# Kernel optimization log

Measured on AMD Instinct MI355X. Metric: run time of the kernel, lower is better.

## Reference

```python
import jax, jax.numpy as jnp
import numpy as np

B, S = 4, 2048
D_MODEL, N_HEADS, D_KV = 1024, 16, 64
NUM_BUCKETS, MAX_DIST = 32, 128


def _relative_position_bucket(relative_position, num_buckets=NUM_BUCKETS, max_distance=MAX_DIST):
    # bidirectional (encoder) variant, faithful to FlaxT5Attention._relative_position_bucket
    num_buckets = num_buckets // 2
    relative_buckets = (relative_position > 0).astype(jnp.int32) * num_buckets
    rp = jnp.abs(relative_position)
    max_exact = num_buckets // 2
    is_small = rp < max_exact
    rp_large = max_exact + (
        jnp.log(rp.astype(jnp.float32) / max_exact)
        / np.log(max_distance / max_exact)
        * (num_buckets - max_exact)
    )
    rp_large = jnp.minimum(rp_large, num_buckets - 1)
    return relative_buckets + jnp.where(is_small, rp, rp_large.astype(jnp.int32))


def setup_inputs() -> dict:
    key = jax.random.key(0)
    ks = jax.random.split(key, 6)
    return {
        "hidden_states": jax.random.normal(ks[0], (B, S, D_MODEL), jnp.float32),
        "mask": jnp.zeros((B, S), jnp.float32),  # additive mask, 0 = attend
        "wq": jax.random.normal(ks[1], (D_MODEL, N_HEADS * D_KV), jnp.float32) * 0.02,
        "wk": jax.random.normal(ks[2], (D_MODEL, N_HEADS * D_KV), jnp.float32) * 0.02,
        "wv": jax.random.normal(ks[3], (D_MODEL, N_HEADS * D_KV), jnp.float32) * 0.02,
        "wo": jax.random.normal(ks[4], (N_HEADS * D_KV, D_MODEL), jnp.float32) * 0.02,
        "rel_bias": jax.random.normal(ks[5], (NUM_BUCKETS, N_HEADS), jnp.float32) * 0.02,
    }


def reference(hidden_states, mask, wq, wk, wv, wo, rel_bias):
    b, s, _ = hidden_states.shape
    # QKV projections, split heads -> [B, S, H, D]
    q = (hidden_states @ wq).reshape(b, s, N_HEADS, D_KV)
    k = (hidden_states @ wk).reshape(b, s, N_HEADS, D_KV)
    v = (hidden_states @ wv).reshape(b, s, N_HEADS, D_KV)

    # relative position bias -> [1, H, S, S]
    pos = jnp.arange(s, dtype=jnp.int32)
    relative_position = pos[None, :] - pos[:, None]  # memory - query
    buckets = _relative_position_bucket(relative_position)
    position_bias = rel_bias[buckets].transpose(2, 0, 1)[None]  # [1,H,S,S]
    # encoder path: additive mask expanded to [B,1,1,K]
    position_bias = position_bias + mask[:, None, None, :]

    # flax dot_product_attention_weights scales q by 1/sqrt(depth)
    scores = jnp.einsum("bqhd,bkhd->bhqk", q / jnp.sqrt(jnp.float32(D_KV)), k)
    attn_weights = jax.nn.softmax(scores + position_bias, axis=-1)

    attn_output = jnp.einsum("bhqk,bkhd->bqhd", attn_weights, v)
    attn_output = attn_output.reshape(b, s, N_HEADS * D_KV) @ wo
    return attn_output, position_bias
```

## Files before the change

kernel.cpp:

```cpp
#include <hip/hip_runtime.h>
#include <hip/hip_bf16.h>

typedef __attribute__((ext_vector_type(8))) short bf16x8;
typedef __attribute__((ext_vector_type(8))) unsigned short u16x8;
typedef __attribute__((ext_vector_type(4))) float f32x4;

#define B_   4
#define S_   2048
#define H_   16
#define DKV  64
#define DM   1024

static __device__ __forceinline__ f32x4 mfma16(bf16x8 a, bf16x8 b, f32x4 c){
  return __builtin_amdgcn_mfma_f32_16x16x32_bf16(a, b, c, 0, 0, 0);
}
static __device__ __forceinline__ void gload_lds16(const void* g, void* l){
  __builtin_amdgcn_global_load_lds((const __attribute__((address_space(1))) void*)g,
                                   (__attribute__((address_space(3))) void*)l, 16, 0, 0);
}
static __device__ __forceinline__ unsigned short f2b(float f){
  union { __hip_bfloat16 b; unsigned short u; } x;
  x.b = __float2bfloat16(f);
  return x.u;
}

__global__ void cast_h_kernel(const float* __restrict__ in, unsigned short* __restrict__ out, int n4){
  int i = blockIdx.x * 256 + threadIdx.x;
  if (i >= n4) return;
  float4 v = reinterpret_cast<const float4*>(in)[i];
  ushort4 r;
  r.x = f2b(v.x); r.y = f2b(v.y); r.z = f2b(v.z); r.w = f2b(v.w);
  reinterpret_cast<ushort4*>(out)[i] = r;
}

__global__ void transpose_w_kernel(const float* __restrict__ w0, const float* __restrict__ w1,
                                   const float* __restrict__ w2, const float* __restrict__ w3,
                                   unsigned short* o0, unsigned short* o1,
                                   unsigned short* o2, unsigned short* o3){
  int z = blockIdx.z;
  const float* src = (z==0) ? w0 : (z==1) ? w1 : (z==2) ? w2 : w3;
  unsigned short* dst = (z==0) ? o0 : (z==1) ? o1 : (z==2) ? o2 : o3;
  __shared__ float tile[32][33];
  int bx = blockIdx.x * 32, by = blockIdx.y * 32;
  int tx = threadIdx.x, ty = threadIdx.y;
  #pragma unroll
  for (int i = 0; i < 32; i += 8)
    tile[ty + i][tx] = src[(size_t)(by + ty + i) * DM + bx + tx];
  __syncthreads();
  #pragma unroll
  for (int i = 0; i < 32; i += 8)
    dst[(size_t)(bx + ty + i) * DM + by + tx] = f2b(tile[tx][ty + i]);
}

__global__ void build_table_kernel(const float* __restrict__ rel_bias, float* __restrict__ table_t){
  int i = blockIdx.x * 256 + threadIdx.x;
  if (i >= 16 * 4095) return;
  int h = i / 4095;
  int idx = i - h * 4095;
  int rel = idx - 2047;
  int bucket = (rel > 0) ? 16 : 0;
  int rp = (rel < 0) ? -rel : rel;
  int off;
  if (rp < 8) off = rp;
  else off = 8 + (rp>=12) + (rp>=16) + (rp>=23) + (rp>=32) + (rp>=46) + (rp>=64) + (rp>=91);
  table_t[i] = rel_bias[(bucket + off) * 16 + h];
}

__global__ void posbias_kernel(const float* __restrict__ relb, const float* __restrict__ mask,
                               float* __restrict__ out){
  __shared__ float rbh[32];
  int row = blockIdx.x;
  int q = row & (S_ - 1);
  int h = (row >> 11) & (H_ - 1);
  int b = row >> 15;
  int tid = threadIdx.x;
  if (tid < 32) rbh[tid] = relb[tid * 16 + h];
  __syncthreads();
  const float* mrow = mask + b * S_;
  float* orow = out + (size_t)row * S_;
  int k0 = tid * 8;
  #pragma unroll
  for (int c = 0; c < 2; ++c){
    float4 mv = *(const float4*)(mrow + k0 + c * 4);
    float4 v;
    #pragma unroll
    for (int j = 0; j < 4; ++j){
      int k = k0 + c * 4 + j;
      int rel = k - q;
      int bucket = (rel > 0) ? 16 : 0;
      int rp = (rel < 0) ? -rel : rel;
      int off = (rp < 8) ? rp
              : 8 + (rp>=12) + (rp>=16) + (rp>=23) + (rp>=32) + (rp>=46) + (rp>=64) + (rp>=91);
      (&v.x)[j] = rbh[bucket + off] + (&mv.x)[j];
    }
    *(float4*)(orow + k0 + c*4) = v;
  }
}

template<int MODE>
__global__ __launch_bounds__(256, 2) void gemm_bt_kernel(
    const unsigned short* __restrict__ A, const unsigned short* __restrict__ Bt,
    void* __restrict__ outp, int M, int N, int K, float scale)
{
  __shared__ __align__(16) unsigned short As[2][128 * 32];
  __shared__ __align__(16) unsigned short Bs[2][128 * 32];
  int tid = threadIdx.x; int lane = tid & 63; int w = tid >> 6;
  int wr = w >> 1, wc = w & 1;
  int n0 = blockIdx.x * 128, m0 = blockIdx.y * 128;
  const char* Ab = (const char*)A;
  const char* Bb = (const char*)Bt;
  size_t Kb = (size_t)K * 2;

  f32x4 acc[4][4];
  #pragma unroll
  for (int i = 0; i < 4; ++i)
    #pragma unroll
    for (int j = 0; j < 4; ++j) acc[i][j] = (f32x4){0.f, 0.f, 0.f, 0.f};

  auto stage = [&](int kt, int bsel){
    size_t k0b = (size_t)kt * 64;
    #pragma unroll
    for (int c = 0; c < 2; ++c){
      int o = c * 4096 + w * 1024 + lane * 16;
      int row = o >> 6;
      int wbl = (o & 63) ^ (((row >> 1) & 3) << 4);
      gload_lds16(Ab + (size_t)(m0 + row) * Kb + k0b + wbl, (char*)As[bsel] + c * 4096 + w * 1024);
      gload_lds16(Bb + (size_t)(n0 + row) * Kb + k0b + wbl, (char*)Bs[bsel] + c * 4096 + w * 1024);
    }
  };

  int nk = K >> 5;
  int buf = 0;
  stage(0, 0);
  for (int kt = 0; kt < nk; ++kt){
    __syncthreads();
    if (kt + 1 < nk) stage(kt + 1, buf ^ 1);
    bf16x8 af[4], bfr[4];
    #pragma unroll
    for (int f = 0; f < 4; ++f){
      int row = wr * 64 + f * 16 + (lane & 15);
      int byt = (row * 64 + ((lane >> 4) * 16)) ^ (((row >> 1) & 3) << 4);
      af[f] = *(const bf16x8*)((const char*)As[buf] + byt);
    }
    #pragma unroll
    for (int f = 0; f < 4; ++f){
      int row = wc * 64 + f * 16 + (lane & 15);
      int byt = (row * 64 + ((lane >> 4) * 16)) ^ (((row >> 1) & 3) << 4);
      bfr[f] = *(const bf16x8*)((const char*)Bs[buf] + byt);
    }
    #pragma unroll
    for (int i = 0; i < 4; ++i)
      #pragma unroll
      for (int j = 0; j < 4; ++j)
        acc[i][j] = mfma16(af[i], bfr[j], acc[i][j]);
    buf ^= 1;
  }

  #pragma unroll
  for (int i = 0; i < 4; ++i){
    #pragma unroll
    for (int j = 0; j < 4; ++j){
      #pragma unroll
      for (int r = 0; r < 4; ++r){
        int m = m0 + wr * 64 + i * 16 + ((lane >> 4) * 4) + r;
        int n = n0 + wc * 64 + j * 16 + (lane & 15);
        if (MODE == 0){
          ((float*)outp)[(size_t)m * N + n] = acc[i][j][r] * scale;
        } else {
          int sel = n >> 10, nn = n & 1023;
          float v = acc[i][j][r] * (sel == 0 ? 0.125f : 1.0f);
          int b = m >> 11, s = m & 2047, hh = nn >> 6, d = nn & 63;
          ((unsigned short*)outp)[(size_t)sel * 8388608 +
              (((size_t)(b * H_ + hh) * S_) + s) * DKV + d] = f2b(v);
        }
      }
    }
  }
}

__global__ __launch_bounds__(256, 2) void attn_mfma_kernel(
    const unsigned short* __restrict__ Qp, const unsigned short* __restrict__ Kp,
    const unsigned short* __restrict__ Vp, const float* __restrict__ table_t,
    const float* __restrict__ mask, unsigned short* __restrict__ outp)
{
  __shared__ __align__(16) unsigned short Ks[64][72];
  __shared__ __align__(16) unsigned short Vs[64][72];
  __shared__ __align__(16) unsigned short Ps[4][16][72];
  __shared__ float bias_s[127];
  __shared__ float mask_s[64];

  int bid = blockIdx.x;
  int qt = bid & 31; int h = (bid >> 5) & 15; int b = bid >> 9;
  int qb = qt * 64;
  const unsigned short* qptr = Qp + ((size_t)(b * H_ + h) * S_ + qb) * DKV;
  const unsigned short* kptr = Kp + (size_t)(b * H_ + h) * S_ * DKV;
  const unsigned short* vptr = Vp + (size_t)(b * H_ + h) * S_ * DKV;
  int tid = threadIdx.x; int lane = tid & 63; int w = tid >> 6;

  bf16x8 qf[2];
  {
    const unsigned short* qrow = qptr + (size_t)(w * 16 + (lane & 15)) * DKV + 8 * (lane >> 4);
    qf[0] = *(const bf16x8*)qrow;
    qf[1] = *(const bf16x8*)(qrow + 32);
  }
  float l_r[4] = {0.f, 0.f, 0.f, 0.f};
  f32x4 o_acc[4];
  #pragma unroll
  for (int d = 0; d < 4; ++d) o_acc[d] = (f32x4){0.f, 0.f, 0.f, 0.f};

  int bias_base = h * 4095 + (2047 - qb - 63);

  int skey = tid & 63;
  int sd0  = (tid >> 6) * 16;

  u16x8 ka, kb2, va, vb2;
  float biasr = 0.f, maskr = 0.f;
  auto gload = [&](int k0){
    const unsigned short* krow = kptr + (size_t)(k0 + skey) * DKV + sd0;
    const unsigned short* vrow = vptr + (size_t)(k0 + skey) * DKV + sd0;
    ka  = *(const u16x8*)krow;
    kb2 = *(const u16x8*)(krow + 8);
    va  = *(const u16x8*)vrow;
    vb2 = *(const u16x8*)(vrow + 8);
    if (tid < 127) biasr = table_t[bias_base + k0 + tid];
    else if (tid >= 128 && tid < 192) maskr = mask[b * S_ + k0 + (tid - 128)];
  };
  auto lwrite = [&](){
    *(u16x8*)&Ks[skey][sd0]     = ka;
    *(u16x8*)&Ks[skey][sd0 + 8] = kb2;
    #pragma unroll
    for (int j = 0; j < 8; ++j){
      Vs[sd0 + j][skey]     = va[j];
      Vs[sd0 + 8 + j][skey] = vb2[j];
    }
    if (tid < 127) bias_s[tid] = biasr;
    else if (tid < 192) mask_s[tid - 128] = maskr;
  };

  gload(0);
  lwrite();
  for (int k0 = 0; k0 < S_; k0 += 64){
    __syncthreads();
    if (k0 + 64 < S_) gload(k0 + 64);

    f32x4 sc[4];
    #pragma unroll
    for (int kb = 0; kb < 4; ++kb){
      sc[kb] = (f32x4){0.f, 0.f, 0.f, 0.f};
      #pragma unroll
      for (int ks = 0; ks < 2; ++ks){
        int row = kb * 16 + (lane & 15);
        bf16x8 kf = *(const bf16x8*)&Ks[row][ks * 32 + (lane >> 4) * 8];
        sc[kb] = mfma16(qf[ks], kf, sc[kb]);
      }
    }
    float t[4][4];
    float rs[4] = {0.f, 0.f, 0.f, 0.f};
    #pragma unroll
    for (int kb = 0; kb < 4; ++kb){
      int k_l = kb * 16 + (lane & 15);
      float mk = mask_s[k_l];
      #pragma unroll
      for (int r = 0; r < 4; ++r){
        int q_l = w * 16 + (lane >> 4) * 4 + r;
        float p = __expf(sc[kb][r] + bias_s[k_l - q_l + 63] + mk);
        t[kb][r] = p;
        rs[r] += p;
      }
    }
    #pragma unroll
    for (int r = 0; r < 4; ++r){
      #pragma unroll
      for (int off = 1; off < 16; off <<= 1)
        rs[r] += __shfl_xor(rs[r], off, 64);
      l_r[r] += rs[r];
    }
    #pragma unroll
    for (int kb = 0; kb < 4; ++kb)
      #pragma unroll
      for (int r = 0; r < 4; ++r){
        int prow = (lane >> 4) * 4 + r;
        int pcol = kb * 16 + (lane & 15);
        Ps[w][prow][pcol] = f2b(t[kb][r]);
      }
    bf16x8 pa[2];
    #pragma unroll
    for (int ks = 0; ks < 2; ++ks)
      pa[ks] = *(const bf16x8*)&Ps[w][lane & 15][ks * 32 + (lane >> 4) * 8];
    #pragma unroll
    for (int db = 0; db < 4; ++db)
      #pragma unroll
      for (int ks = 0; ks < 2; ++ks){
        bf16x8 vf = *(const bf16x8*)&Vs[db * 16 + (lane & 15)][ks * 32 + (lane >> 4) * 8];
        o_acc[db] = mfma16(pa[ks], vf, o_acc[db]);
      }

    __syncthreads();
    if (k0 + 64 < S_) lwrite();
  }

  #pragma unroll
  for (int r = 0; r < 4; ++r){
    float inv = 1.0f / l_r[r];
    int qg = qb + w * 16 + (lane >> 4) * 4 + r;
    size_t rowoff = ((size_t)b * S_ + qg) * DM + h * DKV;
    #pragma unroll
    for (int db = 0; db < 4; ++db)
      outp[rowoff + db * 16 + (lane & 15)] = f2b(o_acc[db][r] * inv);
  }
}

extern "C" void kernel_launch(void* const* d_in, const int* in_sizes, int n_in,
                              void* d_out, int out_size, void* d_ws, size_t ws_size,
                              hipStream_t stream) {
  const float* hs   = (const float*)d_in[0];
  const float* msk  = (const float*)d_in[1];
  const float* wq   = (const float*)d_in[2];
  const float* wk   = (const float*)d_in[3];
  const float* wv   = (const float*)d_in[4];
  const float* wo   = (const float*)d_in[5];
  const float* relb = (const float*)d_in[6];

  float* out_attn = (float*)d_out;
  float* out_pb   = (float*)d_out + (size_t)B_ * S_ * DM;

  const size_t SCRATCH_NEED = 76021760;
  char* ws = (ws_size >= SCRATCH_NEED && d_ws) ? (char*)d_ws : (char*)out_pb;

  unsigned short* h_bf  = (unsigned short*)(ws + 0);
  unsigned short* wqkv_t= (unsigned short*)(ws + 16777216);
  unsigned short* wk_t  = (unsigned short*)(ws + 18874368);
  unsigned short* wv_t  = (unsigned short*)(ws + 20971520);
  unsigned short* wo_t  = (unsigned short*)(ws + 23068672);
  unsigned short* qkv_b = (unsigned short*)(ws + 25165824);
  unsigned short* k_b   = (unsigned short*)(ws + 41943040);
  unsigned short* v_b   = (unsigned short*)(ws + 58720256);
  float*          tabl  = (float*)(ws + 75497472);

  cast_h_kernel<<<8192, 256, 0, stream>>>(hs, h_bf, (B_ * S_ * DM) / 4);
  transpose_w_kernel<<<dim3(32, 32, 4), dim3(32, 8), 0, stream>>>(wq, wk, wv, wo,
                                                                  wqkv_t, wk_t, wv_t, wo_t);
  build_table_kernel<<<256, 256, 0, stream>>>(relb, tabl);

  gemm_bt_kernel<1><<<dim3(24, 64), 256, 0, stream>>>(h_bf, wqkv_t, qkv_b, 8192, 3072, 1024, 1.0f);

  attn_mfma_kernel<<<B_ * H_ * 32, 256, 0, stream>>>(qkv_b, k_b, v_b, tabl, msk, h_bf);

  gemm_bt_kernel<0><<<dim3(8, 64), 256, 0, stream>>>(h_bf, wo_t, out_attn, 8192, 1024, 1024, 1.0f);

  posbias_kernel<<<B_ * H_ * S_, 256, 0, stream>>>(relb, msk, out_pb);
}
```

Baseline: 502.2 us.

## Process 32 query rows per wave in attention to reuse K/V tiles

The attention kernel now covers 128 queries per block instead of 64, so each wave handles two 16-row query sub-tiles. K and V fragments are loaded from LDS into registers once and reused for both sub-tiles, which halves LDS and global K/V traffic per query. The bias window grows to 191 entries to match. In exchange the grid shrinks to 1024 blocks and register pressure rises, which may lower occupancy under launch_bounds(256,2).

```diff
diff --git a/kernel.cpp b/kernel.cpp
--- a/kernel.cpp
+++ b/kernel.cpp
@@ -185,30 +185,33 @@
 {
   __shared__ __align__(16) unsigned short Ks[64][72];
   __shared__ __align__(16) unsigned short Vs[64][72];
-  __shared__ __align__(16) unsigned short Ps[4][16][72];
-  __shared__ float bias_s[127];
+  __shared__ __align__(16) unsigned short Ps[4][32][72];
+  __shared__ float bias_s[191];
   __shared__ float mask_s[64];
 
   int bid = blockIdx.x;
-  int qt = bid & 31; int h = (bid >> 5) & 15; int b = bid >> 9;
-  int qb = qt * 64;
+  int qt = bid & 15; int h = (bid >> 4) & 15; int b = bid >> 8;
+  int qb = qt * 128;
   const unsigned short* qptr = Qp + ((size_t)(b * H_ + h) * S_ + qb) * DKV;
   const unsigned short* kptr = Kp + (size_t)(b * H_ + h) * S_ * DKV;
   const unsigned short* vptr = Vp + (size_t)(b * H_ + h) * S_ * DKV;
   int tid = threadIdx.x; int lane = tid & 63; int w = tid >> 6;
 
-  bf16x8 qf[2];
-  {
-    const unsigned short* qrow = qptr + (size_t)(w * 16 + (lane & 15)) * DKV + 8 * (lane >> 4);
-    qf[0] = *(const bf16x8*)qrow;
-    qf[1] = *(const bf16x8*)(qrow + 32);
-  }
-  float l_r[4] = {0.f, 0.f, 0.f, 0.f};
-  f32x4 o_acc[4];
-  #pragma unroll
-  for (int d = 0; d < 4; ++d) o_acc[d] = (f32x4){0.f, 0.f, 0.f, 0.f};
-
-  int bias_base = h * 4095 + (2047 - qb - 63);
+  bf16x8 qf[2][2];
+  #pragma unroll
+  for (int qs = 0; qs < 2; ++qs){
+    const unsigned short* qrow = qptr + (size_t)(w * 32 + qs * 16 + (lane & 15)) * DKV + 8 * (lane >> 4);
+    qf[qs][0] = *(const bf16x8*)qrow;
+    qf[qs][1] = *(const bf16x8*)(qrow + 32);
+  }
+  float l_r[2][4] = {{0.f,0.f,0.f,0.f},{0.f,0.f,0.f,0.f}};
+  f32x4 o_acc[2][4];
+  #pragma unroll
+  for (int qs = 0; qs < 2; ++qs)
+    #pragma unroll
+    for (int d = 0; d < 4; ++d) o_acc[qs][d] = (f32x4){0.f, 0.f, 0.f, 0.f};
+
+  int bias_base = h * 4095 + (2047 - qb - 127);
 
   int skey = tid & 63;
   int sd0  = (tid >> 6) * 16;
@@ -222,8 +225,8 @@
     kb2 = *(const u16x8*)(krow + 8);
     va  = *(const u16x8*)vrow;
     vb2 = *(const u16x8*)(vrow + 8);
-    if (tid < 127) biasr = table_t[bias_base + k0 + tid];
-    else if (tid >= 128 && tid < 192) maskr = mask[b * S_ + k0 + (tid - 128)];
+    if (tid < 191) biasr = table_t[bias_base + k0 + tid];
+    else if (tid >= 192) maskr = mask[b * S_ + k0 + (tid - 192)];
   };
   auto lwrite = [&](){
     *(u16x8*)&Ks[skey][sd0]     = ka;
@@ -233,8 +236,8 @@
       Vs[sd0 + j][skey]     = va[j];
       Vs[sd0 + 8 + j][skey] = vb2[j];
     }
-    if (tid < 127) bias_s[tid] = biasr;
-    else if (tid < 192) mask_s[tid - 128] = maskr;
+    if (tid < 191) bias_s[tid] = biasr;
+    else if (tid >= 192) mask_s[tid - 192] = maskr;
   };
 
   gload(0);
@@ -243,71 +246,89 @@
     __syncthreads();
     if (k0 + 64 < S_) gload(k0 + 64);
 
-    f32x4 sc[4];
-    #pragma unroll
-    for (int kb = 0; kb < 4; ++kb){
-      sc[kb] = (f32x4){0.f, 0.f, 0.f, 0.f};
-      #pragma unroll
-      for (int ks = 0; ks < 2; ++ks){
-        int row = kb * 16 + (lane & 15);
-        bf16x8 kf = *(const bf16x8*)&Ks[row][ks * 32 + (lane >> 4) * 8];
-        sc[kb] = mfma16(qf[ks], kf, sc[kb]);
+    bf16x8 kf[4][2];
+    #pragma unroll
+    for (int kb = 0; kb < 4; ++kb)
+      #pragma unroll
+      for (int ks = 0; ks < 2; ++ks)
+        kf[kb][ks] = *(const bf16x8*)&Ks[kb * 16 + (lane & 15)][ks * 32 + (lane >> 4) * 8];
+
+    float t[2][4][4];
+    float rs[2][4] = {{0.f,0.f,0.f,0.f},{0.f,0.f,0.f,0.f}};
+    #pragma unroll
+    for (int qs = 0; qs < 2; ++qs){
+      f32x4 sc[4];
+      #pragma unroll
+      for (int kb = 0; kb < 4; ++kb){
+        sc[kb] = (f32x4){0.f, 0.f, 0.f, 0.f};
+        #pragma unroll
+        for (int ks = 0; ks < 2; ++ks)
+          sc[kb] = mfma16(qf[qs][ks], kf[kb][ks], sc[kb]);
       }
-    }
-    float t[4][4];
-    float rs[4] = {0.f, 0.f, 0.f, 0.f};
-    #pragma unroll
-    for (int kb = 0; kb < 4; ++kb){
-      int k_l = kb * 16 + (lane & 15);
-      float mk = mask_s[k_l];
+      #pragma unroll
+      for (int kb = 0; kb < 4; ++kb){
+        int k_l = kb * 16 + (lane & 15);
+        float mk = mask_s[k_l];
+        #pragma unroll
+        for (int r = 0; r < 4; ++r){
+          int q_l = w * 32 + qs * 16 + (lane >> 4) * 4 + r;
+          float p = __expf(sc[kb][r] + bias_s[k_l - q_l + 127] + mk);
+          t[qs][kb][r] = p;
+          rs[qs][r] += p;
+        }
+      }
+    }
+    #pragma unroll
+    for (int qs = 0; qs < 2; ++qs)
       #pragma unroll
       for (int r = 0; r < 4; ++r){
-        int q_l = w * 16 + (lane >> 4) * 4 + r;
-        float p = __expf(sc[kb][r] + bias_s[k_l - q_l + 63] + mk);
-        t[kb][r] = p;
-        rs[r] += p;
+        #pragma unroll
+        for (int off = 1; off < 16; off <<= 1)
+          rs[qs][r] += __shfl_xor(rs[qs][r], off, 64);
+        l_r[qs][r] += rs[qs][r];
       }
-    }
-    #pragma unroll
-    for (int r = 0; r < 4; ++r){
-      #pragma unroll
-      for (int off = 1; off < 16; off <<= 1)
-        rs[r] += __shfl_xor(rs[r], off, 64);
-      l_r[r] += rs[r];
-    }
-    #pragma unroll
-    for (int kb = 0; kb < 4; ++kb)
-      #pragma unroll
-      for (int r = 0; r < 4; ++r){
-        int prow = (lane >> 4) * 4 + r;
-        int pcol = kb * 16 + (lane & 15);
-        Ps[w][prow][pcol] = f2b(t[kb][r]);
-      }
-    bf16x8 pa[2];
-    #pragma unroll
-    for (int ks = 0; ks < 2; ++ks)
-      pa[ks] = *(const bf16x8*)&Ps[w][lane & 15][ks * 32 + (lane >> 4) * 8];
+    #pragma unroll
+    for (int qs = 0; qs < 2; ++qs)
+      #pragma unroll
+      for (int kb = 0; kb < 4; ++kb)
+        #pragma unroll
+        for (int r = 0; r < 4; ++r)
+          Ps[w][qs * 16 + (lane >> 4) * 4 + r][kb * 16 + (lane & 15)] = f2b(t[qs][kb][r]);
+
+    bf16x8 vf[4][2];
     #pragma unroll
     for (int db = 0; db < 4; ++db)
       #pragma unroll
-      for (int ks = 0; ks < 2; ++ks){
-        bf16x8 vf = *(const bf16x8*)&Vs[db * 16 + (lane & 15)][ks * 32 + (lane >> 4) * 8];
-        o_acc[db] = mfma16(pa[ks], vf, o_acc[db]);
-      }
+      for (int ks = 0; ks < 2; ++ks)
+        vf[db][ks] = *(const bf16x8*)&Vs[db * 16 + (lane & 15)][ks * 32 + (lane >> 4) * 8];
+    #pragma unroll
+    for (int qs = 0; qs < 2; ++qs){
+      bf16x8 pa[2];
+      #pragma unroll
+      for (int ks = 0; ks < 2; ++ks)
+        pa[ks] = *(const bf16x8*)&Ps[w][qs * 16 + (lane & 15)][ks * 32 + (lane >> 4) * 8];
+      #pragma unroll
+      for (int db = 0; db < 4; ++db)
+        #pragma unroll
+        for (int ks = 0; ks < 2; ++ks)
+          o_acc[qs][db] = mfma16(pa[ks], vf[db][ks], o_acc[qs][db]);
+    }
 
     __syncthreads();
     if (k0 + 64 < S_) lwrite();
   }
 
   #pragma unroll
-  for (int r = 0; r < 4; ++r){
-    float inv = 1.0f / l_r[r];
-    int qg = qb + w * 16 + (lane >> 4) * 4 + r;
-    size_t rowoff = ((size_t)b * S_ + qg) * DM + h * DKV;
-    #pragma unroll
-    for (int db = 0; db < 4; ++db)
-      outp[rowoff + db * 16 + (lane & 15)] = f2b(o_acc[db][r] * inv);
-  }
+  for (int qs = 0; qs < 2; ++qs)
+    #pragma unroll
+    for (int r = 0; r < 4; ++r){
+      float inv = 1.0f / l_r[qs][r];
+      int qg = qb + w * 32 + qs * 16 + (lane >> 4) * 4 + r;
+      size_t rowoff = ((size_t)b * S_ + qg) * DM + h * DKV;
+      #pragma unroll
+      for (int db = 0; db < 4; ++db)
+        outp[rowoff + db * 16 + (lane & 15)] = f2b(o_acc[qs][db][r] * inv);
+    }
 }
 
 extern "C" void kernel_launch(void* const* d_in, const int* in_sizes, int n_in,
@@ -344,7 +365,7 @@
 
   gemm_bt_kernel<1><<<dim3(24, 64), 256, 0, stream>>>(h_bf, wqkv_t, qkv_b, 8192, 3072, 1024, 1.0f);
 
-  attn_mfma_kernel<<<B_ * H_ * 32, 256, 0, stream>>>(qkv_b, k_b, v_b, tabl, msk, h_bf);
+  attn_mfma_kernel<<<B_ * H_ * 16, 256, 0, stream>>>(qkv_b, k_b, v_b, tabl, msk, h_bf);
 
   gemm_bt_kernel<0><<<dim3(8, 64), 256, 0, stream>>>(h_bf, wo_t, out_attn, 8192, 1024, 1024, 1.0f);
 
```

New measurement: 484.5 us. -3.5%, faster.
